# Optimization experiments

Measured on AMD Instinct MI355X. Metric: run time of the kernel, lower is better.

Reference implementation:

```python
import jax, jax.numpy as jnp
import numpy as np

C = 1024
H = 16
EPS = 1e-5


def setup_inputs() -> dict:
    key = jax.random.key(0)
    ks = jax.random.split(key, 10)
    B, S = 2, 2048
    s = 1.0 / np.sqrt(C)
    return {
        "hidden_states": jax.random.normal(ks[0], (B, C, S), dtype=jnp.float32),
        "attention_mask": jnp.ones((B, S), dtype=jnp.int32),
        "gn_weight": jnp.ones((C,), dtype=jnp.float32),
        "gn_bias": jnp.zeros((C,), dtype=jnp.float32),
        "Wq": jax.random.normal(ks[1], (C, C), dtype=jnp.float32) * s,
        "bq": jnp.zeros((C,), dtype=jnp.float32),
        "Wk": jax.random.normal(ks[2], (C, C), dtype=jnp.float32) * s,
        "bk": jnp.zeros((C,), dtype=jnp.float32),
        "Wv": jax.random.normal(ks[3], (C, C), dtype=jnp.float32) * s,
        "bv": jnp.zeros((C,), dtype=jnp.float32),
        "Wo": jax.random.normal(ks[4], (C, C), dtype=jnp.float32) * s,
        "bo": jnp.zeros((C,), dtype=jnp.float32),
    }


def reference(hidden_states, attention_mask, gn_weight, gn_bias,
              Wq, bq, Wk, bk, Wv, bv, Wo, bo):
    # hidden_states: (B, C, S); attention_mask: (B, S)
    B, Cc, S = hidden_states.shape
    D = Cc // H
    residual = hidden_states

    # GroupNorm with 1 group: normalize over (C, S) per sample
    mean = jnp.mean(hidden_states, axis=(1, 2), keepdims=True)
    var = jnp.var(hidden_states, axis=(1, 2), keepdims=True)
    x = (hidden_states - mean) * jax.lax.rsqrt(var + EPS)
    x = x * gn_weight[None, :, None] + gn_bias[None, :, None]

    x = jnp.transpose(x, (0, 2, 1))  # (B, S, C)
    q = x @ Wq.T + bq
    k = x @ Wk.T + bk
    v = x @ Wv.T + bv

    # (B, H, S, D)
    q = q.reshape(B, S, H, D).transpose(0, 2, 1, 3)
    k = k.reshape(B, S, H, D).transpose(0, 2, 1, 3)
    v = v.reshape(B, S, H, D).transpose(0, 2, 1, 3)

    scale = 1.0 / np.sqrt(np.sqrt(D))
    scores = jnp.einsum('bhqd,bhkd->bhqk', q * scale, k * scale)
    mask = attention_mask[:, None, None, :]  # (B,1,1,S) broadcast over heads/query
    scores = jnp.where(mask == 0, -jnp.inf, scores)
    probs = jax.nn.softmax(scores, axis=-1)

    out = jnp.einsum('bhqk,bhkd->bhqd', probs, v)  # (B,H,S,D)
    out = out.transpose(0, 2, 1, 3).reshape(B, S, Cc)
    out = out @ Wo.T + bo
    out = jnp.transpose(out, (0, 2, 1))  # (B, C, S)
    return out + residual
```

## Files before the change

kernel.cpp:

```cpp
#include <hip/hip_runtime.h>
#include <hip/hip_bf16.h>

#define B_ 2
#define C_ 1024
#define S_ 2048
#define H_ 16
#define KDIM 1024

typedef __attribute__((ext_vector_type(8))) short short8_t;
typedef __attribute__((ext_vector_type(4))) float f32x4;
typedef __attribute__((ext_vector_type(16))) float f32x16;
typedef __attribute__((ext_vector_type(4))) int i32x4;

__device__ __forceinline__ void glds16(const void* g, void* l) {
  __builtin_amdgcn_global_load_lds((const __attribute__((address_space(1))) void*)g,
                                   (__attribute__((address_space(3))) void*)l, 16, 0, 0);
}

__device__ __forceinline__ unsigned short f2bf(float f) {
  __hip_bfloat16 h = __float2bfloat16(f);
  return __builtin_bit_cast(unsigned short, h);
}

__device__ __forceinline__ unsigned pkbf(float lo, float hi) {
  unsigned r;
  asm("v_cvt_pk_bf16_f32 %0, %1, %2" : "=v"(r) : "v"(lo), "v"(hi));
  return r;
}

__device__ __forceinline__ void plswap(unsigned &a, unsigned &b) {
  asm("v_permlane32_swap_b32 %0, %1" : "+v"(a), "+v"(b));
}

__device__ __forceinline__ float max16v(const f32x16& v) {
  float a = fmaxf(fmaxf(v[0], v[1]),  fmaxf(v[2], v[3]));
  float b = fmaxf(fmaxf(v[4], v[5]),  fmaxf(v[6], v[7]));
  float c = fmaxf(fmaxf(v[8], v[9]),  fmaxf(v[10], v[11]));
  float d = fmaxf(fmaxf(v[12], v[13]), fmaxf(v[14], v[15]));
  return fmaxf(fmaxf(a, b), fmaxf(c, d));
}

__device__ __forceinline__ float sum16v(const f32x16& p) {
  float a = (p[0] + p[1]) + (p[2] + p[3]);
  float b = (p[4] + p[5]) + (p[6] + p[7]);
  float c = (p[8] + p[9]) + (p[10] + p[11]);
  float d = (p[12] + p[13]) + (p[14] + p[15]);
  return (a + b) + (c + d);
}

__global__ __launch_bounds__(256) void cvt_w4(const float* __restrict__ a,
                                              const float* __restrict__ b,
                                              const float* __restrict__ c,
                                              const float* __restrict__ d,
                                              unsigned short* __restrict__ o) {
  int g = blockIdx.x >> 10;
  const float* src = (g == 0) ? a : (g == 1) ? b : (g == 2) ? c : d;
  int i = (blockIdx.x & 1023) * 256 + threadIdx.x;
  float4 v = ((const float4*)src)[i];
  short4 r;
  r.x = (short)f2bf(v.x); r.y = (short)f2bf(v.y);
  r.z = (short)f2bf(v.z); r.w = (short)f2bf(v.w);
  ((short4*)(o))[(size_t)g * 262144 + i] = r;
}

__global__ __launch_bounds__(256) void stats1(const float* __restrict__ x,
                                              float2* __restrict__ part) {
  int bid = blockIdx.x;
  int b = bid >> 8, chunk = bid & 255;
  const float4* p = (const float4*)(x + (size_t)b*(C_*S_) + (size_t)chunk*8192);
  int t = threadIdx.x;
  float s = 0.f, q = 0.f;
#pragma unroll
  for (int i = 0; i < 8; ++i) {
    float4 v = p[t + i*256];
    s += v.x + v.y + v.z + v.w;
    q += v.x*v.x + v.y*v.y + v.z*v.z + v.w*v.w;
  }
#pragma unroll
  for (int d = 1; d < 64; d <<= 1) { s += __shfl_xor(s, d); q += __shfl_xor(q, d); }
  __shared__ float2 wsum[4];
  if ((t & 63) == 0) wsum[t >> 6] = make_float2(s, q);
  __syncthreads();
  if (t == 0) {
    float S = 0.f, Q = 0.f;
    for (int i = 0; i < 4; ++i) { S += wsum[i].x; Q += wsum[i].y; }
    part[bid] = make_float2(S, Q);
  }
}

__global__ __launch_bounds__(256) void stats2(const float2* __restrict__ part,
                                              float* __restrict__ stats) {
  int b = blockIdx.x;
  int t = threadIdx.x;
  float2 v = part[b*256 + t];
  float s = v.x, q = v.y;
#pragma unroll
  for (int d = 1; d < 64; d <<= 1) { s += __shfl_xor(s, d); q += __shfl_xor(q, d); }
  __shared__ float2 wsum[4];
  if ((t & 63) == 0) wsum[t >> 6] = make_float2(s, q);
  __syncthreads();
  if (t == 0) {
    float S = 0.f, Q = 0.f;
    for (int i = 0; i < 4; ++i) { S += wsum[i].x; Q += wsum[i].y; }
    const float invN = 1.0f / (float)(C_*S_);
    float mean = S * invN;
    float var = Q * invN - mean*mean;
    stats[b*2]   = mean;
    stats[b*2+1] = rsqrtf(var + 1e-5f);
  }
}

__global__ __launch_bounds__(256) void normt(const float* __restrict__ x,
                                             const float* __restrict__ gw,
                                             const float* __restrict__ gb,
                                             const float* __restrict__ stats,
                                             unsigned short* __restrict__ xt) {
  __shared__ short lds[64*72];
  int bid = blockIdx.x;
  int b = bid >> 9, rem = bid & 511;
  int ct = rem >> 5, st = rem & 31;
  float mean = stats[b*2], rstd = stats[b*2+1];
  int t = threadIdx.x;
  int r = t >> 2, seg = t & 3;
  int c = ct*64 + r;
  float wsc = gw[c] * rstd;
  float bof = gb[c] - mean * wsc;
  const float4* src = (const float4*)(x + (size_t)b*(C_*S_) + (size_t)c*S_ + st*64 + seg*16);
#pragma unroll
  for (int j = 0; j < 4; ++j) {
    float4 v = src[j];
    int sl = seg*16 + j*4;
    lds[(sl+0)*72 + r] = (short)f2bf(v.x*wsc + bof);
    lds[(sl+1)*72 + r] = (short)f2bf(v.y*wsc + bof);
    lds[(sl+2)*72 + r] = (short)f2bf(v.z*wsc + bof);
    lds[(sl+3)*72 + r] = (short)f2bf(v.w*wsc + bof);
  }
  __syncthreads();
  int sl = t >> 2;
  __attribute__((aligned(16))) unsigned short tmp[16];
#pragma unroll
  for (int j = 0; j < 16; ++j) tmp[j] = (unsigned short)lds[sl*72 + seg*16 + j];
  unsigned short* dst = xt + ((size_t)b*S_ + st*64 + sl) * C_ + ct*64 + seg*16;
  *(short8_t*)dst       = *(const short8_t*)tmp;
  *(short8_t*)(dst + 8) = *(const short8_t*)(tmp + 8);
}

template<int EPI>
__global__ __launch_bounds__(256)
void gemm_nt(const unsigned short* __restrict__ A,
             const unsigned short* __restrict__ Bm,
             const float* __restrict__ bias,
             const float* __restrict__ resid,
             void* __restrict__ outp,
             int nbn) {
  __shared__ __attribute__((aligned(16))) short As[64*64];
  __shared__ __attribute__((aligned(16))) short Bs[128*64];
  int nwg = gridDim.x;
  int bid = blockIdx.x;
  int cpx = nwg >> 3;
  int sbid = (bid & 7) * cpx + (bid >> 3);
  int bm = sbid / nbn, bn = sbid % nbn;
  int m0 = bm << 6, n0 = bn << 7;
  int t = threadIdx.x;
  int l = t & 63, wid = t >> 6;

  int r_st = t >> 3;
  int slot_src = (t & 7) ^ (r_st & 7);
  const unsigned short* a_src = A + (size_t)(m0 + r_st) * KDIM + slot_src * 8;
  const unsigned short* b_src = Bm + (size_t)(n0 + r_st) * KDIM + slot_src * 8;
  char* As_base = (char*)As + wid*1024;
  char* Bs_base = (char*)Bs + wid*1024;

  f32x4 acc[4][2] = {};

  for (int kt = 0; kt < KDIM; kt += 64) {
    __syncthreads();
    glds16(a_src + kt, As_base);
    glds16(a_src + (size_t)32*KDIM + kt, As_base + 4096);
#pragma unroll
    for (int i = 0; i < 4; ++i)
      glds16(b_src + (size_t)(i*32)*KDIM + kt, Bs_base + i*4096);
    __syncthreads();
#pragma unroll
    for (int kk = 0; kk < 2; ++kk) {
      short8_t af[4], bfr[2];
#pragma unroll
      for (int mi = 0; mi < 4; ++mi) {
        int row = mi*16 + (l & 15);
        int slot = (kk*4 + (l >> 4)) ^ (row & 7);
        af[mi] = *(const short8_t*)((const char*)As + row*128 + slot*16);
      }
#pragma unroll
      for (int ni = 0; ni < 2; ++ni) {
        int row = wid*32 + ni*16 + (l & 15);
        int slot = (kk*4 + (l >> 4)) ^ (row & 7);
        bfr[ni] = *(const short8_t*)((const char*)Bs + row*128 + slot*16);
      }
#pragma unroll
      for (int mi = 0; mi < 4; ++mi)
#pragma unroll
        for (int ni = 0; ni < 2; ++ni)
          acc[mi][ni] = __builtin_amdgcn_mfma_f32_16x16x32_bf16(af[mi], bfr[ni], acc[mi][ni], 0, 0, 0);
    }
  }

#pragma unroll
  for (int mi = 0; mi < 4; ++mi) {
#pragma unroll
    for (int ni = 0; ni < 2; ++ni) {
#pragma unroll
      for (int r = 0; r < 4; ++r) {
        int gm = m0 + mi*16 + ((l >> 4) << 2) + r;
        int gn = n0 + wid*32 + ni*16 + (l & 15);
        float v = acc[mi][ni][r];
        if (EPI == 0) {
          v += bias[gn];
          size_t off = ((size_t)((gm >> 11)*H_ + (gn >> 6)) * S_ + (gm & 2047)) * 64 + (gn & 63);
          ((unsigned short*)outp)[off] = f2bf(v);
        } else {
          v += bias[gm];
          size_t off = (size_t)(gn >> 11) * ((size_t)C_*S_) + (size_t)gm * S_ + (gn & 2047);
          if (EPI == 1) {
            ((unsigned short*)outp)[off] = f2bf(v);
          } else {
            ((float*)outp)[off] = v + resid[off];
          }
        }
      }
    }
  }
}

__global__ __launch_bounds__(512, 4)
void attn_kernel(const unsigned short* __restrict__ Q,
                 const unsigned short* __restrict__ Kt,
                 const unsigned short* __restrict__ Vt,
                 const int* __restrict__ mask,
                 unsigned short* __restrict__ outp) {
  __shared__ __attribute__((aligned(16))) char lds[65536];
  __shared__ __attribute__((aligned(8)))  unsigned char maskb[256];
  __shared__ int tflag[32];

  int bid = blockIdx.x;
  int bid2 = (bid & 7) * 64 + (bid >> 3);
  int bh = bid2 >> 4, qt = bid2 & 15;
  int b = bh >> 4, h = bh & 15;
  int t = threadIdx.x, l = t & 63, wid = t >> 6;
  int quad = wid >> 2, qw = wid & 3;
  int hh = l >> 5;

  if (t < 256) {
    const i32x4* mp = (const i32x4*)(mask + b * S_) + t * 2;
    i32x4 m0 = mp[0], m1 = mp[1];
    unsigned by = (unsigned)(m0[0]!=0) | ((unsigned)(m0[1]!=0)<<1) | ((unsigned)(m0[2]!=0)<<2) | ((unsigned)(m0[3]!=0)<<3)
                | ((unsigned)(m1[0]!=0)<<4) | ((unsigned)(m1[1]!=0)<<5) | ((unsigned)(m1[2]!=0)<<6) | ((unsigned)(m1[3]!=0)<<7);
    maskb[t] = (unsigned char)by;
  }
  __syncthreads();
  if (t < 32) {
    unsigned long long v = ((const unsigned long long*)maskb)[t];
    tflag[t] = (v == 0xFFFFFFFFFFFFFFFFull) ? 1 : 0;
  }

  int q0 = qt*128 + qw*32;
  const unsigned short* qp = Q + ((size_t)bh * S_ + q0 + (l & 31)) * 64 + hh * 8;
  short8_t qf[4];
#pragma unroll
  for (int c = 0; c < 4; ++c) qf[c] = *(const short8_t*)(qp + c*16);

  int kbase = quad << 10;
  int row_st = qw*16 + (l >> 3);
  int slot_st = (l & 7) ^ (l >> 3);
  const unsigned short* kp = Kt + ((size_t)bh * S_ + kbase + row_st) * 64 + slot_st * 8;
  const unsigned short* vp = Vt + ((size_t)bh * 64 + row_st) * S_ + kbase + slot_st * 8;
  char* kdst = lds + quad*16384 + qw*2048;
  char* vdst = kdst + 32768;

  unsigned ko[8];
#pragma unroll
  for (int c = 0; c < 4; ++c) {
    unsigned slot = (unsigned)((c*2 + hh) ^ (l & 7)) * 16u;
    ko[c]   = (unsigned)(quad*16384) + (unsigned)(l & 31)*128u + slot;
    ko[c+4] = ko[c] + 4096u;
  }

  const float SC = 0.18033688011112042f;
  float m_run = 0.f, msc = 0.f, l_run = 0.f;
  f32x16 oc0 = {}, oc1 = {};

  glds16(kp,                kdst);
  glds16(kp + 8*64,         kdst + 1024);
  glds16(vp,                vdst);
  glds16(vp + (size_t)8*S_, vdst + 1024);
  const unsigned short* kn = kp + 64*64;
  const unsigned short* vn = vp + 64;
  int lt = 0;

#define ATILE(BUF)                                                              \
  do {                                                                          \
    __syncthreads();                                                            \
    glds16(kn,                kdst + ((BUF)^1)*8192);                           \
    glds16(kn + 8*64,         kdst + ((BUF)^1)*8192 + 1024);                    \
    glds16(vn,                vdst + ((BUF)^1)*8192);                           \
    glds16(vn + (size_t)8*S_, vdst + ((BUF)^1)*8192 + 1024);                    \
    kn += 4096; vn += 64;                                                       \
    f32x16 st0 = {}, st1 = {};                                                  \
    __builtin_amdgcn_s_setprio(1);                                              \
    _Pragma("unroll")                                                           \
    for (int c = 0; c < 4; ++c) {                                               \
      short8_t kf0 = *(const short8_t*)(lds + ko[c]   + (BUF)*8192);            \
      short8_t kf1 = *(const short8_t*)(lds + ko[c+4] + (BUF)*8192);            \
      st0 = __builtin_amdgcn_mfma_f32_32x32x16_bf16(kf0, qf[c], st0, 0, 0, 0);  \
      st1 = __builtin_amdgcn_mfma_f32_32x32x16_bf16(kf1, qf[c], st1, 0, 0, 0);  \
    }                                                                           \
    __builtin_amdgcn_s_setprio(0);                                              \
    _Pragma("unroll")                                                           \
    for (int r = 0; r < 16; ++r) {                                              \
      st0[r] = __builtin_amdgcn_exp2f(fmaf(st0[r], SC, -msc));                  \
      st1[r] = __builtin_amdgcn_exp2f(fmaf(st1[r], SC, -msc));                  \
    }                                                                           \
    if (!tflag[(kbase >> 6) + lt]) {                                            \
      _Pragma("unroll")                                                         \
      for (int r = 0; r < 16; ++r) {                                            \
        int kl = kbase + lt*64 + (r & 3) + 8*(r >> 2) + 4*hh;                   \
        if (!((maskb[kl >> 3] >> (kl & 7)) & 1)) st0[r] = 0.f;                  \
        kl += 32;                                                               \
        if (!((maskb[kl >> 3] >> (kl & 7)) & 1)) st1[r] = 0.f;                  \
      }                                                                         \
    }                                                                           \
    float pmax = fmaxf(max16v(st0), max16v(st1));                               \
    l_run += sum16v(st0) + sum16v(st1);                                         \
    short8_t pa[4];                                                             \
    {                                                                           \
      unsigned a0 = pkbf(st0[0],  st0[1]),  b0 = pkbf(st0[4],  st0[5]);         \
      unsigned a1 = pkbf(st0[2],  st0[3]),  b1 = pkbf(st0[6],  st0[7]);         \
      plswap(a0, b0); plswap(a1, b1);                                           \
      i32x4 w0 = {(int)a0, (int)a1, (int)b0, (int)b1};                          \
      pa[0] = __builtin_bit_cast(short8_t, w0);                                 \
      unsigned a2 = pkbf(st0[8],  st0[9]),  b2 = pkbf(st0[12], st0[13]);        \
      unsigned a3 = pkbf(st0[10], st0[11]), b3 = pkbf(st0[14], st0[15]);        \
      plswap(a2, b2); plswap(a3, b3);                                           \
      i32x4 w1 = {(int)a2, (int)a3, (int)b2, (int)b3};                          \
      pa[1] = __builtin_bit_cast(short8_t, w1);                                 \
      unsigned a4 = pkbf(st1[0],  st1[1]),  b4 = pkbf(st1[4],  st1[5]);         \
      unsigned a5 = pkbf(st1[2],  st1[3]),  b5 = pkbf(st1[6],  st1[7]);         \
      plswap(a4, b4); plswap(a5, b5);                                           \
      i32x4 w2 = {(int)a4, (int)a5, (int)b4, (int)b5};                          \
      pa[2] = __builtin_bit_cast(short8_t, w2);                                 \
      unsigned a6 = pkbf(st1[8],  st1[9]),  b6 = pkbf(st1[12], st1[13]);        \
      unsigned a7 = pkbf(st1[10], st1[11]), b7 = pkbf(st1[14], st1[15]);        \
      plswap(a6, b6); plswap(a7, b7);                                           \
      i32x4 w3 = {(int)a6, (int)a7, (int)b6, (int)b7};                          \
      pa[3] = __builtin_bit_cast(short8_t, w3);                                 \
    }                                                                           \
    __builtin_amdgcn_s_setprio(1);                                              \
    _Pragma("unroll")                                                           \
    for (int kc = 0; kc < 4; ++kc) {                                            \
      short8_t vf0 = *(const short8_t*)(lds + ko[kc]   + 32768 + (BUF)*8192);   \
      short8_t vf1 = *(const short8_t*)(lds + ko[kc+4] + 32768 + (BUF)*8192);   \
      oc0 = __builtin_amdgcn_mfma_f32_32x32x16_bf16(vf0, pa[kc], oc0, 0, 0, 0); \
      oc1 = __builtin_amdgcn_mfma_f32_32x32x16_bf16(vf1, pa[kc], oc1, 0, 0, 0); \
    }                                                                           \
    __builtin_amdgcn_s_setprio(0);                                              \
    if (__any(pmax > 148.0f)) {                                                 \
      float pm = fmaxf(pmax, __shfl_xor(pmax, 32));                             \
      float smax = (__log2f(pm) + msc) / SC;                                    \
      float nm = fmaxf(m_run, smax);                                            \
      float fac = __builtin_amdgcn_exp2f((m_run - nm) * SC);                    \
      _Pragma("unroll")                                                         \
      for (int r = 0; r < 16; ++r) { oc0[r] *= fac; oc1[r] *= fac; }            \
      l_run *= fac; m_run = nm; msc = nm * SC;                                  \
    }                                                                           \
    ++lt;                                                                       \
  } while (0)

  for (int tp = 0; tp < 8; ++tp) {
    ATILE(0);
    ATILE(1);
  }
#undef ATILE

  __syncthreads();
  if (quad == 1) {
    char* obuf = lds + qw*8192 + l*128;
#pragma unroll
    for (int j = 0; j < 4; ++j) {
      f32x4 u0 = { oc0[4*j], oc0[4*j+1], oc0[4*j+2], oc0[4*j+3] };
      *(f32x4*)(obuf + ((j ^ (l & 7)) * 16)) = u0;
      f32x4 u1 = { oc1[4*j], oc1[4*j+1], oc1[4*j+2], oc1[4*j+3] };
      *(f32x4*)(obuf + (((j+4) ^ (l & 7)) * 16)) = u1;
    }
    *(float2*)(lds + 32768 + (qw*64 + l)*8) = make_float2(l_run, m_run);
  }
  __syncthreads();
  if (quad == 0) {
    float2 lm1 = *(const float2*)(lds + 32768 + (qw*64 + l)*8);
    float M  = fmaxf(m_run, lm1.y);
    float a0 = __builtin_amdgcn_exp2f((m_run - M) * SC);
    float a1 = __builtin_amdgcn_exp2f((lm1.y - M) * SC);
    float lc = l_run * a0 + lm1.x * a1;
    float ltot = lc + __shfl_xor(lc, 32);
    float inv = 1.f / ltot;
    float s0 = a0 * inv, s1 = a1 * inv;
    const char* obuf = lds + qw*8192 + l*128;
#pragma unroll
    for (int j = 0; j < 4; ++j) {
      f32x4 u0 = *(const f32x4*)(obuf + ((j ^ (l & 7)) * 16));
      oc0[4*j]   = oc0[4*j]  *s0 + u0[0]*s1;
      oc0[4*j+1] = oc0[4*j+1]*s0 + u0[1]*s1;
      oc0[4*j+2] = oc0[4*j+2]*s0 + u0[2]*s1;
      oc0[4*j+3] = oc0[4*j+3]*s0 + u0[3]*s1;
      f32x4 u1 = *(const f32x4*)(obuf + (((j+4) ^ (l & 7)) * 16));
      oc1[4*j]   = oc1[4*j]  *s0 + u1[0]*s1;
      oc1[4*j+1] = oc1[4*j+1]*s0 + u1[1]*s1;
      oc1[4*j+2] = oc1[4*j+2]*s0 + u1[2]*s1;
      oc1[4*j+3] = oc1[4*j+3]*s0 + u1[3]*s1;
    }

    unsigned short* obase = outp + ((size_t)b * S_ + q0 + (l & 31)) * C_ + h*64 + hh*8;
#pragma unroll
    for (int dt = 0; dt < 2; ++dt) {
      const f32x16& oc = dt ? oc1 : oc0;
      unsigned a0w = pkbf(oc[0],  oc[1]),  b0w = pkbf(oc[4],  oc[5]);
      unsigned a1w = pkbf(oc[2],  oc[3]),  b1w = pkbf(oc[6],  oc[7]);
      plswap(a0w, b0w); plswap(a1w, b1w);
      i32x4 w0 = {(int)a0w, (int)a1w, (int)b0w, (int)b1w};
      *(i32x4*)(obase + dt*32) = w0;
      unsigned a2w = pkbf(oc[8],  oc[9]),  b2w = pkbf(oc[12], oc[13]);
      unsigned a3w = pkbf(oc[10], oc[11]), b3w = pkbf(oc[14], oc[15]);
      plswap(a2w, b2w); plswap(a3w, b3w);
      i32x4 w1 = {(int)a2w, (int)a3w, (int)b2w, (int)b3w};
      *(i32x4*)(obase + dt*32 + 16) = w1;
    }
  }
}

extern "C" void kernel_launch(void* const* d_in, const int* in_sizes, int n_in,
                              void* d_out, int out_size, void* d_ws, size_t ws_size,
                              hipStream_t stream) {
  const float* hs = (const float*)d_in[0];
  const int*   msk = (const int*)d_in[1];
  const float* gw = (const float*)d_in[2];
  const float* gb = (const float*)d_in[3];
  const float* Wq = (const float*)d_in[4];
  const float* bq = (const float*)d_in[5];
  const float* Wk = (const float*)d_in[6];
  const float* bk = (const float*)d_in[7];
  const float* Wv = (const float*)d_in[8];
  const float* bv = (const float*)d_in[9];
  const float* Wo = (const float*)d_in[10];
  const float* bo = (const float*)d_in[11];

  char* ws = (char*)d_ws;
  float*  stats = (float*)(ws);
  float2* part  = (float2*)(ws + 256);
  unsigned short* wq_b = (unsigned short*)(ws + 8192);
  unsigned short* wk_b = wq_b + 1048576;
  unsigned short* wv_b = wk_b + 1048576;
  unsigned short* wo_b = wv_b + 1048576;
  unsigned short* x_b  = wo_b + 1048576;
  unsigned short* q_b  = x_b  + 4194304;
  unsigned short* k_b  = q_b  + 4194304;
  unsigned short* vt_b = k_b  + 4194304;
  unsigned short* ao_b = vt_b + 4194304;

  cvt_w4<<<4096, 256, 0, stream>>>(Wq, Wk, Wv, Wo, wq_b);

  stats1<<<512, 256, 0, stream>>>(hs, part);
  stats2<<<2, 256, 0, stream>>>(part, stats);
  normt<<<1024, 256, 0, stream>>>(hs, gw, gb, stats, x_b);

  gemm_nt<0><<<512, 256, 0, stream>>>(x_b, wq_b, bq, nullptr, q_b, 8);
  gemm_nt<0><<<512, 256, 0, stream>>>(x_b, wk_b, bk, nullptr, k_b, 8);
  gemm_nt<1><<<512, 256, 0, stream>>>(wv_b, x_b, bv, nullptr, vt_b, 32);

  attn_kernel<<<512, 512, 0, stream>>>(q_b, k_b, vt_b, msk, ao_b);

  gemm_nt<2><<<512, 256, 0, stream>>>(wo_b, ao_b, bo, hs, d_out, 32);
}
```

Baseline: 134.1 us.

## Fuse Q/K projections into one GEMM, use MFMA row sums and max3 in attention

Q and K projections now run as a single 128x128-tiled GEMM over the concatenated Wq/Wk weights, which are contiguous in the workspace. This replaces two launches and reuses each X tile for both outputs. In attention, the softmax denominator now comes from an extra MFMA against a ones vector, replacing the scalar sum16 reduction and the cross-lane shuffle. The row max now uses v_max3. The trade is extra MFMA work and accumulator registers in the attention inner loop, plus a larger-tile GEMM that may reduce occupancy.

After: 124.1 us. 7.5% less time.

```diff
diff --git a/kernel.cpp b/kernel.cpp
--- a/kernel.cpp
+++ b/kernel.cpp
@@ -32,20 +32,21 @@
   asm("v_permlane32_swap_b32 %0, %1" : "+v"(a), "+v"(b));
 }
 
+__device__ __forceinline__ float max3f(float a, float b, float c) {
+  float r;
+  asm("v_max3_f32 %0, %1, %2, %3" : "=v"(r) : "v"(a), "v"(b), "v"(c));
+  return r;
+}
+
 __device__ __forceinline__ float max16v(const f32x16& v) {
-  float a = fmaxf(fmaxf(v[0], v[1]),  fmaxf(v[2], v[3]));
-  float b = fmaxf(fmaxf(v[4], v[5]),  fmaxf(v[6], v[7]));
-  float c = fmaxf(fmaxf(v[8], v[9]),  fmaxf(v[10], v[11]));
-  float d = fmaxf(fmaxf(v[12], v[13]), fmaxf(v[14], v[15]));
-  return fmaxf(fmaxf(a, b), fmaxf(c, d));
-}
-
-__device__ __forceinline__ float sum16v(const f32x16& p) {
-  float a = (p[0] + p[1]) + (p[2] + p[3]);
-  float b = (p[4] + p[5]) + (p[6] + p[7]);
-  float c = (p[8] + p[9]) + (p[10] + p[11]);
-  float d = (p[12] + p[13]) + (p[14] + p[15]);
-  return (a + b) + (c + d);
+  float a = max3f(v[0], v[1], v[2]);
+  float b = max3f(v[3], v[4], v[5]);
+  float c = max3f(v[6], v[7], v[8]);
+  float d = max3f(v[9], v[10], v[11]);
+  float e = max3f(v[12], v[13], v[14]);
+  float f = max3f(a, b, v[15]);
+  float g = max3f(c, d, e);
+  return fmaxf(f, g);
 }
 
 __global__ __launch_bounds__(256) void cvt_w4(const float* __restrict__ a,
@@ -143,6 +144,79 @@
   unsigned short* dst = xt + ((size_t)b*S_ + st*64 + sl) * C_ + ct*64 + seg*16;
   *(short8_t*)dst       = *(const short8_t*)tmp;
   *(short8_t*)(dst + 8) = *(const short8_t*)(tmp + 8);
+}
+
+__global__ __launch_bounds__(256)
+void gemm_qk(const unsigned short* __restrict__ A,
+             const unsigned short* __restrict__ Bm,
+             const float* __restrict__ bq,
+             const float* __restrict__ bk,
+             unsigned short* __restrict__ outp) {
+  __shared__ __attribute__((aligned(16))) short As[128*64];
+  __shared__ __attribute__((aligned(16))) short Bs[128*64];
+  int bid = blockIdx.x;
+  int sbid = (bid & 7) * 64 + (bid >> 3);
+  int bm = sbid >> 4, bn = sbid & 15;
+  int m0 = bm << 7, n0 = bn << 7;
+  int t = threadIdx.x, l = t & 63, wid = t >> 6;
+  int wr = wid >> 1, wc = wid & 1;
+
+  int rsb = wid*8 + (l >> 3);
+  int slot_src = (l & 7) ^ (l >> 3);
+  const unsigned short* a_src = A + (size_t)(m0 + rsb) * KDIM + slot_src * 8;
+  const unsigned short* b_src = Bm + (size_t)(n0 + rsb) * KDIM + slot_src * 8;
+  char* adst = (char*)As + wid*1024;
+  char* bdst = (char*)Bs + wid*1024;
+
+  f32x4 acc[4][4] = {};
+
+  for (int kt = 0; kt < KDIM; kt += 64) {
+    __syncthreads();
+#pragma unroll
+    for (int i = 0; i < 4; ++i) {
+      glds16(a_src + (size_t)(i*32)*KDIM + kt, adst + i*4096);
+      glds16(b_src + (size_t)(i*32)*KDIM + kt, bdst + i*4096);
+    }
+    __syncthreads();
+#pragma unroll
+    for (int kk = 0; kk < 2; ++kk) {
+      short8_t af[4], bf[4];
+#pragma unroll
+      for (int mi = 0; mi < 4; ++mi) {
+        int row = wr*64 + mi*16 + (l & 15);
+        int slot = (kk*4 + (l >> 4)) ^ (row & 7);
+        af[mi] = *(const short8_t*)((const char*)As + row*128 + slot*16);
+      }
+#pragma unroll
+      for (int ni = 0; ni < 4; ++ni) {
+        int row = wc*64 + ni*16 + (l & 15);
+        int slot = (kk*4 + (l >> 4)) ^ (row & 7);
+        bf[ni] = *(const short8_t*)((const char*)Bs + row*128 + slot*16);
+      }
+#pragma unroll
+      for (int mi = 0; mi < 4; ++mi)
+#pragma unroll
+        for (int ni = 0; ni < 4; ++ni)
+          acc[mi][ni] = __builtin_amdgcn_mfma_f32_16x16x32_bf16(af[mi], bf[ni], acc[mi][ni], 0, 0, 0);
+    }
+  }
+
+  int gcol0 = n0 + wc*64;
+  const float* bp = (gcol0 & 1024) ? bk : bq;
+  unsigned short* ob = outp + ((gcol0 & 1024) ? 4194304u : 0u);
+  int hd0 = gcol0 & 1023;
+#pragma unroll
+  for (int mi = 0; mi < 4; ++mi)
+#pragma unroll
+    for (int ni = 0; ni < 4; ++ni)
+#pragma unroll
+      for (int r = 0; r < 4; ++r) {
+        int gm = m0 + wr*64 + mi*16 + ((l >> 4) << 2) + r;
+        int hd = hd0 + ni*16 + (l & 15);
+        float v = acc[mi][ni][r] + bp[hd];
+        size_t off = ((size_t)((gm >> 11)*H_ + (hd >> 6)) * S_ + (gm & 2047)) * 64 + (hd & 63);
+        ob[off] = f2bf(v);
+      }
 }
 
 template<int EPI>
@@ -213,18 +287,12 @@
         int gm = m0 + mi*16 + ((l >> 4) << 2) + r;
         int gn = n0 + wid*32 + ni*16 + (l & 15);
         float v = acc[mi][ni][r];
-        if (EPI == 0) {
-          v += bias[gn];
-          size_t off = ((size_t)((gm >> 11)*H_ + (gn >> 6)) * S_ + (gm & 2047)) * 64 + (gn & 63);
+        v += bias[gm];
+        size_t off = (size_t)(gn >> 11) * ((size_t)C_*S_) + (size_t)gm * S_ + (gn & 2047);
+        if (EPI == 1) {
           ((unsigned short*)outp)[off] = f2bf(v);
         } else {
-          v += bias[gm];
-          size_t off = (size_t)(gn >> 11) * ((size_t)C_*S_) + (size_t)gm * S_ + (gn & 2047);
-          if (EPI == 1) {
-            ((unsigned short*)outp)[off] = f2bf(v);
-          } else {
-            ((float*)outp)[off] = v + resid[off];
-          }
+          ((float*)outp)[off] = v + resid[off];
         }
       }
     }
@@ -284,9 +352,10 @@
     ko[c+4] = ko[c] + 4096u;
   }
 
+  const short8_t vones = {0x3F80, 0x3F80, 0x3F80, 0x3F80, 0x3F80, 0x3F80, 0x3F80, 0x3F80};
   const float SC = 0.18033688011112042f;
-  float m_run = 0.f, msc = 0.f, l_run = 0.f;
-  f32x16 oc0 = {}, oc1 = {};
+  float m_run = 0.f, msc = 0.f;
+  f32x16 oc0 = {}, oc1 = {}, lsum = {};
 
   glds16(kp,                kdst);
   glds16(kp + 8*64,         kdst + 1024);
@@ -329,7 +398,6 @@
       }                                                                         \
     }                                                                           \
     float pmax = fmaxf(max16v(st0), max16v(st1));                               \
-    l_run += sum16v(st0) + sum16v(st1);                                         \
     short8_t pa[4];                                                             \
     {                                                                           \
       unsigned a0 = pkbf(st0[0],  st0[1]),  b0 = pkbf(st0[4],  st0[5]);         \
@@ -360,6 +428,7 @@
       short8_t vf1 = *(const short8_t*)(lds + ko[kc+4] + 32768 + (BUF)*8192);   \
       oc0 = __builtin_amdgcn_mfma_f32_32x32x16_bf16(vf0, pa[kc], oc0, 0, 0, 0); \
       oc1 = __builtin_amdgcn_mfma_f32_32x32x16_bf16(vf1, pa[kc], oc1, 0, 0, 0); \
+      lsum = __builtin_amdgcn_mfma_f32_32x32x16_bf16(vones, pa[kc], lsum, 0, 0, 0); \
     }                                                                           \
     __builtin_amdgcn_s_setprio(0);                                              \
     if (__any(pmax > 148.0f)) {                                                 \
@@ -368,8 +437,8 @@
       float nm = fmaxf(m_run, smax);                                            \
       float fac = __builtin_amdgcn_exp2f((m_run - nm) * SC);                    \
       _Pragma("unroll")                                                         \
-      for (int r = 0; r < 16; ++r) { oc0[r] *= fac; oc1[r] *= fac; }            \
-      l_run *= fac; m_run = nm; msc = nm * SC;                                  \
+      for (int r = 0; r < 16; ++r) { oc0[r] *= fac; oc1[r] *= fac; lsum[r] *= fac; } \
+      m_run = nm; msc = nm * SC;                                                \
     }                                                                           \
     ++lt;                                                                       \
   } while (0)
@@ -390,7 +459,7 @@
       f32x4 u1 = { oc1[4*j], oc1[4*j+1], oc1[4*j+2], oc1[4*j+3] };
       *(f32x4*)(obuf + (((j+4) ^ (l & 7)) * 16)) = u1;
     }
-    *(float2*)(lds + 32768 + (qw*64 + l)*8) = make_float2(l_run, m_run);
+    *(float2*)(lds + 32768 + (qw*64 + l)*8) = make_float2(lsum[0], m_run);
   }
   __syncthreads();
   if (quad == 0) {
@@ -398,9 +467,8 @@
     float M  = fmaxf(m_run, lm1.y);
     float a0 = __builtin_amdgcn_exp2f((m_run - M) * SC);
     float a1 = __builtin_amdgcn_exp2f((lm1.y - M) * SC);
-    float lc = l_run * a0 + lm1.x * a1;
-    float ltot = lc + __shfl_xor(lc, 32);
-    float inv = 1.f / ltot;
+    float lc = lsum[0] * a0 + lm1.x * a1;
+    float inv = 1.f / lc;
     float s0 = a0 * inv, s1 = a1 * inv;
     const char* obuf = lds + qw*8192 + l*128;
 #pragma unroll
@@ -470,8 +538,7 @@
   stats2<<<2, 256, 0, stream>>>(part, stats);
   normt<<<1024, 256, 0, stream>>>(hs, gw, gb, stats, x_b);
 
-  gemm_nt<0><<<512, 256, 0, stream>>>(x_b, wq_b, bq, nullptr, q_b, 8);
-  gemm_nt<0><<<512, 256, 0, stream>>>(x_b, wk_b, bk, nullptr, k_b, 8);
+  gemm_qk<<<512, 256, 0, stream>>>(x_b, wq_b, bq, bk, q_b);
   gemm_nt<1><<<512, 256, 0, stream>>>(wv_b, x_b, bv, nullptr, vt_b, 32);
 
   attn_kernel<<<512, 512, 0, stream>>>(q_b, k_b, vt_b, msk, ao_b);
```
